# Kernel tuning notes

Measured on AMD Instinct MI355X. Metric: run time of the kernel, lower is better.

## Reference

```python
import jax, jax.numpy as jnp
import numpy as np

B, C_IN, C_OUT, PODS = 32, 128, 128, 2
H_IN, W_IN = 56, 56
H_PAD, W_PAD = 64, 64  # next powers of 2


def hadamard_matrix(n):
    # Sylvester construction; n is a power of 2 (fixed small loop over log2 n)
    H = jnp.array([[1.0]], dtype=jnp.float32)
    base = jnp.array([[1.0, 1.0], [1.0, -1.0]], dtype=jnp.float32)
    for _ in range(int(np.log2(n))):
        H = jnp.kron(H, base)
    return H


def setup_inputs() -> dict:
    key = jax.random.key(0)
    k1, k2, k3, k4 = jax.random.split(key, 4)
    x = jax.random.normal(k1, (B, C_IN, H_IN, W_IN), dtype=jnp.float32)
    # grouped 1x1 conv weight, one (out,in) matrix per pod
    conv_w = jax.random.normal(k2, (PODS, C_OUT, C_IN), dtype=jnp.float32) / np.sqrt(C_IN)
    log_v = jnp.zeros((PODS, H_PAD, W_PAD), dtype=jnp.float32)
    T = jax.random.uniform(k3, (C_OUT, 1, 1), dtype=jnp.float32) / 10.0
    return {"x": x, "conv_w": conv_w, "log_v": log_v, "T": T}


def reference(x, conv_w, log_v, T):
    Hh = hadamard_matrix(H_PAD)  # symmetric
    Hw = hadamard_matrix(W_PAD)
    # pad spatial dims up to powers of 2
    f0 = jnp.pad(x, ((0, 0), (0, 0), (0, H_PAD - H_IN), (0, W_PAD - W_IN)))
    # WHT along W then H (H is symmetric so u @ H == H @ u along that axis)
    f1 = jnp.einsum('bchw,wk->bchk', f0, Hw)
    f2 = jnp.einsum('bchw,hk->bckw', f1, Hh)
    # per-pod frequency-domain scaling: (B,pods,C,H,W)
    v = jnp.exp(log_v)  # (pods,H,W)
    f2e = f2[:, None] * v[None, :, None]
    # grouped 1x1 conv (one GEMM per pod) + sum over pods
    f5 = jnp.einsum('bpihw,poi->bohw', f2e, conv_w)
    # per-channel soft thresholding
    thr = jax.nn.relu(T)  # (C_out,1,1)
    f6 = jnp.copysign(jax.nn.relu(jnp.abs(f5) - thr), f5)
    # inverse WHT (divide by n per axis)
    f7 = jnp.einsum('bchw,wk->bchk', f6, Hw) / W_PAD
    f8 = jnp.einsum('bchw,hk->bckw', f7, Hh) / H_PAD
    y = f8[..., :H_IN, :W_IN]
    # residual (C_in == C_out)
    return y + x
```

## Files before the change

kernel.cpp:

```cpp
#include <hip/hip_runtime.h>
#include <hip/hip_bf16.h>

using bf16x8  = __attribute__((ext_vector_type(8))) short;
using f32x4   = __attribute__((ext_vector_type(4))) float;
using ushort8 = __attribute__((ext_vector_type(8))) unsigned short;

#define BB   32
#define CIN  128
#define COUT 128
#define PODS 2
#define HIN  56
#define WIN  56
#define HW   4096

__device__ __forceinline__ unsigned short bf16bits(float v) {
  __hip_bfloat16 h = __float2bfloat16(v);
  return reinterpret_cast<unsigned short&>(h);
}
__device__ __forceinline__ float bits2f(unsigned short u) {
  return __uint_as_float(((unsigned)u) << 16);
}

template<int LEN>
__device__ __forceinline__ void fwht_stage(float (&a)[64]) {
  #pragma unroll
  for (int i = 0; i < 64; i += 2*LEN) {
    #pragma unroll
    for (int j = 0; j < LEN; ++j) {
      float u = a[i+j], v = a[i+j+LEN];
      a[i+j]     = u + v;
      a[i+j+LEN] = u - v;
    }
  }
}
__device__ __forceinline__ void fwht64(float (&a)[64]) {
  fwht_stage<1>(a); fwht_stage<2>(a); fwht_stage<4>(a);
  fwht_stage<8>(a); fwht_stage<16>(a); fwht_stage<32>(a);
}

#define LDS_WAIT() asm volatile("s_waitcnt lgkmcnt(0)" ::: "memory")

__global__ __launch_bounds__(64) void k_fwht_fwd(const float* __restrict__ x,
                                                 unsigned short* __restrict__ F) {
  const int wg   = blockIdx.x;
  const int bc   = (wg & 7)*512 + (wg >> 3);
  const int lane = threadIdx.x;

  __shared__ __align__(16) char smem[64*68*4];
  float (*t)[68] = reinterpret_cast<float(*)[68]>(smem);

  float a[64];
  #pragma unroll
  for (int h = 0; h < 64; ++h) a[h] = 0.f;
  if (lane < WIN) {
    const float* xp = x + (size_t)bc*(HIN*WIN) + lane;
    #pragma unroll
    for (int h = 0; h < HIN; ++h) a[h] = xp[h*WIN];
  }

  fwht64(a);

  #pragma unroll
  for (int k = 0; k < 64; ++k) t[k][lane] = a[k];
  LDS_WAIT();
  #pragma unroll
  for (int w4 = 0; w4 < 16; ++w4) {
    float4 v = *reinterpret_cast<const float4*>(&t[lane][w4*4]);
    a[w4*4+0] = v.x; a[w4*4+1] = v.y; a[w4*4+2] = v.z; a[w4*4+3] = v.w;
  }

  fwht64(a);

  #pragma unroll
  for (int j = 0; j < 8; ++j) {
    ushort8 v;
    #pragma unroll
    for (int e = 0; e < 8; ++e) v[e] = bf16bits(a[j*8 + e]);
    *reinterpret_cast<ushort8*>(&smem[lane*128 + ((j*16) ^ ((lane&7)<<4))]) = v;
  }
  LDS_WAIT();

  unsigned short* Fp = F + (size_t)bc * HW;
  #pragma unroll
  for (int jj = 0; jj < 8; ++jj) {
    int r     = jj*8 + (lane >> 3);
    int inner = (lane & 7) * 16;
    ushort8 v = *reinterpret_cast<const ushort8*>(&smem[r*128 + (inner ^ ((r&7)<<4))]);
    *reinterpret_cast<ushort8*>(Fp + jj*512 + lane*8) = v;
  }
}

__global__ __launch_bounds__(256, 3) void k_mix(const unsigned short* F,
                                                const float* __restrict__ cw,
                                                const float* __restrict__ lv,
                                                const float* __restrict__ T,
                                                unsigned short* G) {
  const int wg   = blockIdx.x;
  const int swz  = (wg & 7)*128 + (wg >> 3);
  const int b    = swz >> 5;
  const int hwb  = swz & 31;
  const int tid  = threadIdx.x;
  const int wv   = tid >> 6;
  const int l    = tid & 63;

  __shared__ __align__(16) char FT[32768];
  __shared__ float ev[PODS][128];

  {
    int p = tid >> 7, h = tid & 127;
    ev[p][h] = expf(lv[p*HW + hwb*128 + h]);
  }

  {
    const unsigned short* Fb = F + (size_t)b*CIN*HW + hwb*128 + 2*l;
    const int i0w = wv*32;
    unsigned uu[32];
    #pragma unroll
    for (int i = 0; i < 32; ++i)
      uu[i] = *reinterpret_cast<const unsigned*>(Fb + (size_t)(i0w + i)*HW);
    const int r0 = 2*l, r1 = 2*l + 1;
    #pragma unroll
    for (int m = 0; m < 4; ++m) {
      ushort8 v0, v1;
      #pragma unroll
      for (int e = 0; e < 8; ++e) {
        unsigned u = uu[m*8 + e];
        v0[e] = (unsigned short)(u & 0xffffu);
        v1[e] = (unsigned short)(u >> 16);
      }
      int colb = wv*64 + m*16;
      *reinterpret_cast<ushort8*>(&FT[r0*256 + (colb ^ ((r0&15)<<4))]) = v0;
      *reinterpret_cast<ushort8*>(&FT[r1*256 + (colb ^ ((r1&15)<<4))]) = v1;
    }
  }

  bf16x8 afr[PODS][2][4];
  {
    const int g8 = (l >> 4) * 8;
    #pragma unroll
    for (int p = 0; p < PODS; ++p)
      #pragma unroll
      for (int tm = 0; tm < 2; ++tm)
        #pragma unroll
        for (int kk = 0; kk < 4; ++kk) {
          int o = wv*32 + tm*16 + (l & 15);
          const float* wp = cw + ((size_t)(p*COUT + o))*CIN + kk*32 + g8;
          float4 w0 = *reinterpret_cast<const float4*>(wp);
          float4 w1 = *reinterpret_cast<const float4*>(wp + 4);
          bf16x8 fr;
          fr[0] = (short)bf16bits(w0.x); fr[1] = (short)bf16bits(w0.y);
          fr[2] = (short)bf16bits(w0.z); fr[3] = (short)bf16bits(w0.w);
          fr[4] = (short)bf16bits(w1.x); fr[5] = (short)bf16bits(w1.y);
          fr[6] = (short)bf16bits(w1.z); fr[7] = (short)bf16bits(w1.w);
          afr[p][tm][kk] = fr;
        }
  }

  float th[2][4];
  #pragma unroll
  for (int tm = 0; tm < 2; ++tm)
    #pragma unroll
    for (int r = 0; r < 4; ++r)
      th[tm][r] = fmaxf(T[wv*32 + tm*16 + (l >> 4)*4 + r], 0.f);

  __syncthreads();

  unsigned short* Gb = G + (size_t)b * COUT * HW + hwb*128;

  #pragma unroll
  for (int t = 0; t < 8; ++t) {
    f32x4 acc[2][2];
    #pragma unroll
    for (int tm = 0; tm < 2; ++tm)
      #pragma unroll
      for (int p = 0; p < PODS; ++p)
        acc[tm][p] = (f32x4){0.f, 0.f, 0.f, 0.f};

    const int row = t*16 + (l & 15);
    const int rb  = row << 8;
    const int sw  = (row & 15) << 4;
    #pragma unroll
    for (int kk = 0; kk < 4; ++kk) {
      int cb = (kk*64 + (l >> 4)*16) ^ sw;
      bf16x8 bfrag = *reinterpret_cast<const bf16x8*>(&FT[rb + cb]);
      #pragma unroll
      for (int tm = 0; tm < 2; ++tm) {
        acc[tm][0] = __builtin_amdgcn_mfma_f32_16x16x32_bf16(afr[0][tm][kk], bfrag, acc[tm][0], 0, 0, 0);
        acc[tm][1] = __builtin_amdgcn_mfma_f32_16x16x32_bf16(afr[1][tm][kk], bfrag, acc[tm][1], 0, 0, 0);
      }
    }

    const float v0 = ev[0][t*16 + (l & 15)];
    const float v1 = ev[1][t*16 + (l & 15)];
    #pragma unroll
    for (int tm = 0; tm < 2; ++tm) {
      #pragma unroll
      for (int r = 0; r < 4; ++r) {
        float f = v0*acc[tm][0][r] + v1*acc[tm][1][r];
        float m = fabsf(f) - th[tm][r];
        m = m > 0.f ? m : 0.f;
        int o = wv*32 + tm*16 + (l >> 4)*4 + r;
        Gb[(size_t)o*HW + t*16 + (l & 15)] = bf16bits(copysignf(m, f));
      }
    }
  }
}

__global__ __launch_bounds__(64) void k_ifwht(const unsigned short* __restrict__ G,
                                              const unsigned short* __restrict__ F,
                                              float* __restrict__ y) {
  const int wg   = blockIdx.x;
  const int bo   = (wg & 7)*512 + (wg >> 3);
  const int lane = threadIdx.x;

  __shared__ __align__(16) char smem[64*68*4];
  float (*t)[68] = reinterpret_cast<float(*)[68]>(smem);

  const unsigned short* Gp = G + (size_t)bo * HW;
  const unsigned short* Fp = F + (size_t)bo * HW;
  #pragma unroll
  for (int jj = 0; jj < 8; ++jj) {
    ushort8 g = *reinterpret_cast<const ushort8*>(Gp + jj*512 + lane*8);
    ushort8 f = *reinterpret_cast<const ushort8*>(Fp + jj*512 + lane*8);
    int kh  = jj*8 + (lane >> 3);
    int kw0 = (lane & 7) * 8;
    float4 lo = {bits2f(g[0]) + bits2f(f[0]), bits2f(g[1]) + bits2f(f[1]),
                 bits2f(g[2]) + bits2f(f[2]), bits2f(g[3]) + bits2f(f[3])};
    float4 hi = {bits2f(g[4]) + bits2f(f[4]), bits2f(g[5]) + bits2f(f[5]),
                 bits2f(g[6]) + bits2f(f[6]), bits2f(g[7]) + bits2f(f[7])};
    *reinterpret_cast<float4*>(&t[kh][kw0])     = lo;
    *reinterpret_cast<float4*>(&t[kh][kw0 + 4]) = hi;
  }
  LDS_WAIT();

  float a[64];
  #pragma unroll
  for (int kh = 0; kh < 64; ++kh) a[kh] = t[kh][lane];

  fwht64(a);

  #pragma unroll
  for (int h = 0; h < 64; ++h) t[h][lane] = a[h];
  LDS_WAIT();
  #pragma unroll
  for (int w4 = 0; w4 < 16; ++w4) {
    float4 v = *reinterpret_cast<const float4*>(&t[lane][w4*4]);
    a[w4*4+0] = v.x; a[w4*4+1] = v.y; a[w4*4+2] = v.z; a[w4*4+3] = v.w;
  }

  fwht64(a);

  #pragma unroll
  for (int w4 = 0; w4 < 16; ++w4) {
    float4 v = {a[w4*4+0]*(1.f/4096.f), a[w4*4+1]*(1.f/4096.f),
                a[w4*4+2]*(1.f/4096.f), a[w4*4+3]*(1.f/4096.f)};
    *reinterpret_cast<float4*>(&t[lane][w4*4]) = v;
  }
  LDS_WAIT();

  if (lane < WIN) {
    float* yp = y + (size_t)bo*(HIN*WIN) + lane;
    #pragma unroll
    for (int h = 0; h < HIN; ++h) {
      yp[h*WIN] = t[h][lane];
    }
  }
}

extern "C" void kernel_launch(void* const* d_in, const int* in_sizes, int n_in,
                              void* d_out, int out_size, void* d_ws, size_t ws_size,
                              hipStream_t stream) {
  const float* x  = (const float*)d_in[0];
  const float* cw = (const float*)d_in[1];
  const float* lv = (const float*)d_in[2];
  const float* T  = (const float*)d_in[3];
  float* y = (float*)d_out;

  char* ws = (char*)d_ws;
  const size_t szF = (size_t)BB * CIN * HW * 2;
  const size_t szG = (size_t)BB * COUT * HW * 2;

  unsigned short* F  = (unsigned short*)ws;
  unsigned short* G  = (unsigned short*)(ws + szF);
  (void)ws_size;

  k_fwht_fwd<<<dim3(BB*CIN),  dim3(64),  0, stream>>>(x, F);
  k_mix     <<<dim3(BB*32),   dim3(256), 0, stream>>>(F, cw, lv, T, G);
  k_ifwht   <<<dim3(BB*COUT), dim3(64),  0, stream>>>(G, F, y);
}
```

Measured before the change: 73.64 us.

## Shrink LDS to bf16 transposes, pack FWHT in float2, raise occupancy

The forward and inverse WHT kernels now stage their transposes through LDS as bf16 with a 144-byte padded row stride, which cuts shared memory per block roughly in half. The butterflies operate on float2 vectors so the compiler can emit packed FP32 adds. Launch bounds now request 4 waves per SIMD, and the block-index swizzle is removed. The inverse kernel writes its output in two halves through a smaller float buffer. The cost is an extra bf16 rounding between the two transform passes, which reduces accuracy.

```diff
diff --git a/kernel.cpp b/kernel.cpp
--- a/kernel.cpp
+++ b/kernel.cpp
@@ -2,6 +2,7 @@
 #include <hip/hip_bf16.h>
 
 using bf16x8  = __attribute__((ext_vector_type(8))) short;
+using f32x2   = __attribute__((ext_vector_type(2))) float;
 using f32x4   = __attribute__((ext_vector_type(4))) float;
 using ushort8 = __attribute__((ext_vector_type(8))) unsigned short;
 
@@ -21,71 +22,74 @@
   return __uint_as_float(((unsigned)u) << 16);
 }
 
-template<int LEN>
-__device__ __forceinline__ void fwht_stage(float (&a)[64]) {
-  #pragma unroll
-  for (int i = 0; i < 64; i += 2*LEN) {
-    #pragma unroll
-    for (int j = 0; j < LEN; ++j) {
-      float u = a[i+j], v = a[i+j+LEN];
-      a[i+j]     = u + v;
-      a[i+j+LEN] = u - v;
-    }
-  }
-}
-__device__ __forceinline__ void fwht64(float (&a)[64]) {
-  fwht_stage<1>(a); fwht_stage<2>(a); fwht_stage<4>(a);
-  fwht_stage<8>(a); fwht_stage<16>(a); fwht_stage<32>(a);
+__device__ __forceinline__ void fwht64v(f32x2 (&a)[32]) {
+  #pragma unroll
+  for (int i = 0; i < 32; ++i) {
+    float u = a[i][0], v = a[i][1];
+    a[i][0] = u + v; a[i][1] = u - v;
+  }
+  #pragma unroll
+  for (int d = 1; d <= 16; d <<= 1) {
+    #pragma unroll
+    for (int i = 0; i < 32; i += 2*d) {
+      #pragma unroll
+      for (int j = 0; j < d; ++j) {
+        f32x2 u = a[i+j], v = a[i+j+d];
+        a[i+j]   = u + v;
+        a[i+j+d] = u - v;
+      }
+    }
+  }
 }
 
 #define LDS_WAIT() asm volatile("s_waitcnt lgkmcnt(0)" ::: "memory")
 
-__global__ __launch_bounds__(64) void k_fwht_fwd(const float* __restrict__ x,
-                                                 unsigned short* __restrict__ F) {
-  const int wg   = blockIdx.x;
-  const int bc   = (wg & 7)*512 + (wg >> 3);
+__global__ __launch_bounds__(64, 4) void k_fwht_fwd(const float* __restrict__ x,
+                                                    unsigned short* __restrict__ F) {
+  const int bc   = blockIdx.x;
   const int lane = threadIdx.x;
 
-  __shared__ __align__(16) char smem[64*68*4];
-  float (*t)[68] = reinterpret_cast<float(*)[68]>(smem);
-
-  float a[64];
-  #pragma unroll
-  for (int h = 0; h < 64; ++h) a[h] = 0.f;
+  __shared__ __align__(16) char smem[64*144];
+
+  f32x2 av[32];
+  #pragma unroll
+  for (int i = 0; i < 32; ++i) av[i] = (f32x2){0.f, 0.f};
   if (lane < WIN) {
     const float* xp = x + (size_t)bc*(HIN*WIN) + lane;
     #pragma unroll
-    for (int h = 0; h < HIN; ++h) a[h] = xp[h*WIN];
-  }
-
-  fwht64(a);
-
-  #pragma unroll
-  for (int k = 0; k < 64; ++k) t[k][lane] = a[k];
-  LDS_WAIT();
-  #pragma unroll
-  for (int w4 = 0; w4 < 16; ++w4) {
-    float4 v = *reinterpret_cast<const float4*>(&t[lane][w4*4]);
-    a[w4*4+0] = v.x; a[w4*4+1] = v.y; a[w4*4+2] = v.z; a[w4*4+3] = v.w;
-  }
-
-  fwht64(a);
+    for (int h = 0; h < HIN; ++h) av[h>>1][h&1] = xp[h*WIN];
+  }
+
+  fwht64v(av);
+
+  #pragma unroll
+  for (int k = 0; k < 64; ++k)
+    *reinterpret_cast<unsigned short*>(&smem[k*144 + lane*2]) = bf16bits(av[k>>1][k&1]);
+  LDS_WAIT();
+  #pragma unroll
+  for (int c = 0; c < 8; ++c) {
+    ushort8 v = *reinterpret_cast<const ushort8*>(&smem[lane*144 + c*16]);
+    #pragma unroll
+    for (int e = 0; e < 8; ++e) av[c*4 + (e>>1)][e&1] = bits2f(v[e]);
+  }
+  LDS_WAIT();
+
+  fwht64v(av);
 
   #pragma unroll
   for (int j = 0; j < 8; ++j) {
     ushort8 v;
     #pragma unroll
-    for (int e = 0; e < 8; ++e) v[e] = bf16bits(a[j*8 + e]);
-    *reinterpret_cast<ushort8*>(&smem[lane*128 + ((j*16) ^ ((lane&7)<<4))]) = v;
+    for (int e = 0; e < 8; ++e) v[e] = bf16bits(av[j*4 + (e>>1)][e&1]);
+    *reinterpret_cast<ushort8*>(&smem[lane*144 + j*16]) = v;
   }
   LDS_WAIT();
 
   unsigned short* Fp = F + (size_t)bc * HW;
   #pragma unroll
   for (int jj = 0; jj < 8; ++jj) {
-    int r     = jj*8 + (lane >> 3);
-    int inner = (lane & 7) * 16;
-    ushort8 v = *reinterpret_cast<const ushort8*>(&smem[r*128 + (inner ^ ((r&7)<<4))]);
+    int r = jj*8 + (lane >> 3);
+    ushort8 v = *reinterpret_cast<const ushort8*>(&smem[r*144 + (lane & 7)*16]);
     *reinterpret_cast<ushort8*>(Fp + jj*512 + lane*8) = v;
   }
 }
@@ -206,15 +210,13 @@
   }
 }
 
-__global__ __launch_bounds__(64) void k_ifwht(const unsigned short* __restrict__ G,
-                                              const unsigned short* __restrict__ F,
-                                              float* __restrict__ y) {
-  const int wg   = blockIdx.x;
-  const int bo   = (wg & 7)*512 + (wg >> 3);
+__global__ __launch_bounds__(64, 4) void k_ifwht(const unsigned short* __restrict__ G,
+                                                 const unsigned short* __restrict__ F,
+                                                 float* __restrict__ y) {
+  const int bo   = blockIdx.x;
   const int lane = threadIdx.x;
 
-  __shared__ __align__(16) char smem[64*68*4];
-  float (*t)[68] = reinterpret_cast<float(*)[68]>(smem);
+  __shared__ __align__(16) char smem[64*144];
 
   const unsigned short* Gp = G + (size_t)bo * HW;
   const unsigned short* Fp = F + (size_t)bo * HW;
@@ -222,48 +224,66 @@
   for (int jj = 0; jj < 8; ++jj) {
     ushort8 g = *reinterpret_cast<const ushort8*>(Gp + jj*512 + lane*8);
     ushort8 f = *reinterpret_cast<const ushort8*>(Fp + jj*512 + lane*8);
-    int kh  = jj*8 + (lane >> 3);
-    int kw0 = (lane & 7) * 8;
-    float4 lo = {bits2f(g[0]) + bits2f(f[0]), bits2f(g[1]) + bits2f(f[1]),
-                 bits2f(g[2]) + bits2f(f[2]), bits2f(g[3]) + bits2f(f[3])};
-    float4 hi = {bits2f(g[4]) + bits2f(f[4]), bits2f(g[5]) + bits2f(f[5]),
-                 bits2f(g[6]) + bits2f(f[6]), bits2f(g[7]) + bits2f(f[7])};
-    *reinterpret_cast<float4*>(&t[kh][kw0])     = lo;
-    *reinterpret_cast<float4*>(&t[kh][kw0 + 4]) = hi;
-  }
-  LDS_WAIT();
-
-  float a[64];
-  #pragma unroll
-  for (int kh = 0; kh < 64; ++kh) a[kh] = t[kh][lane];
-
-  fwht64(a);
-
-  #pragma unroll
-  for (int h = 0; h < 64; ++h) t[h][lane] = a[h];
-  LDS_WAIT();
-  #pragma unroll
-  for (int w4 = 0; w4 < 16; ++w4) {
-    float4 v = *reinterpret_cast<const float4*>(&t[lane][w4*4]);
-    a[w4*4+0] = v.x; a[w4*4+1] = v.y; a[w4*4+2] = v.z; a[w4*4+3] = v.w;
-  }
-
-  fwht64(a);
-
-  #pragma unroll
-  for (int w4 = 0; w4 < 16; ++w4) {
-    float4 v = {a[w4*4+0]*(1.f/4096.f), a[w4*4+1]*(1.f/4096.f),
-                a[w4*4+2]*(1.f/4096.f), a[w4*4+3]*(1.f/4096.f)};
-    *reinterpret_cast<float4*>(&t[lane][w4*4]) = v;
-  }
-  LDS_WAIT();
-
+    int kh = jj*8 + (lane >> 3);
+    ushort8 s;
+    #pragma unroll
+    for (int e = 0; e < 8; ++e) s[e] = bf16bits(bits2f(g[e]) + bits2f(f[e]));
+    *reinterpret_cast<ushort8*>(&smem[kh*144 + (lane & 7)*16]) = s;
+  }
+  LDS_WAIT();
+
+  f32x2 av[32];
+  #pragma unroll
+  for (int k = 0; k < 64; ++k)
+    av[k>>1][k&1] = bits2f(*reinterpret_cast<const unsigned short*>(&smem[k*144 + lane*2]));
+  LDS_WAIT();
+
+  fwht64v(av);
+
+  #pragma unroll
+  for (int h = 0; h < 64; ++h)
+    *reinterpret_cast<unsigned short*>(&smem[h*144 + lane*2]) = bf16bits(av[h>>1][h&1]);
+  LDS_WAIT();
+  #pragma unroll
+  for (int c = 0; c < 8; ++c) {
+    ushort8 v = *reinterpret_cast<const ushort8*>(&smem[lane*144 + c*16]);
+    #pragma unroll
+    for (int e = 0; e < 8; ++e) av[c*4 + (e>>1)][e&1] = bits2f(v[e]);
+  }
+  LDS_WAIT();
+
+  fwht64v(av);
+
+  #pragma unroll
+  for (int i = 0; i < 32; ++i) av[i] *= (1.f/4096.f);
+
+  float (*tf)[72] = reinterpret_cast<float(*)[72]>(smem);
+  float* yp = y + (size_t)bo*(HIN*WIN) + lane;
+
+  if (lane < 32) {
+    #pragma unroll
+    for (int w4 = 0; w4 < 16; ++w4) {
+      float4 v = {av[w4*2][0], av[w4*2][1], av[w4*2+1][0], av[w4*2+1][1]};
+      *reinterpret_cast<float4*>(&tf[lane][w4*4]) = v;
+    }
+  }
+  LDS_WAIT();
   if (lane < WIN) {
-    float* yp = y + (size_t)bo*(HIN*WIN) + lane;
-    #pragma unroll
-    for (int h = 0; h < HIN; ++h) {
-      yp[h*WIN] = t[h][lane];
-    }
+    #pragma unroll
+    for (int h = 0; h < 32; ++h) yp[h*WIN] = tf[h][lane];
+  }
+  LDS_WAIT();
+  if (lane >= 32 && lane < HIN) {
+    #pragma unroll
+    for (int w4 = 0; w4 < 16; ++w4) {
+      float4 v = {av[w4*2][0], av[w4*2][1], av[w4*2+1][0], av[w4*2+1][1]};
+      *reinterpret_cast<float4*>(&tf[lane - 32][w4*4]) = v;
+    }
+  }
+  LDS_WAIT();
+  if (lane < WIN) {
+    #pragma unroll
+    for (int h = 32; h < HIN; ++h) yp[h*WIN] = tf[h - 32][lane];
   }
 }
 
@@ -278,7 +298,6 @@
 
   char* ws = (char*)d_ws;
   const size_t szF = (size_t)BB * CIN * HW * 2;
-  const size_t szG = (size_t)BB * COUT * HW * 2;
 
   unsigned short* F  = (unsigned short*)ws;
   unsigned short* G  = (unsigned short*)(ws + szF);
```

Measured after the change: 70.02 us (median of 2 runs). -4.9%, faster.
